# Performance work log

Measured on AMD Instinct MI355X. Metric: run time of the kernel, lower is better.

The kernel has to match this reference:

```python
import jax, jax.numpy as jnp
import numpy as np

G = 4          # num_groups == num_kv_groups


def _proj(W, b, xf):
    # 1x1 Conv3d == per-voxel linear: xf is [b, c, N]
    return jnp.einsum('oc,bcn->bon', W, xf) + b[None, :, None]


def setup_inputs() -> dict:
    key = jax.random.key(0)
    ks = jax.random.split(key, 5)
    c = 512
    x = jax.random.normal(ks[0], (2, c, 16, 16, 16), dtype=jnp.float32)
    s = 1.0 / np.sqrt(c)
    Wq = jax.random.normal(ks[1], (c, c), dtype=jnp.float32) * s
    Wk = jax.random.normal(ks[2], (c, c), dtype=jnp.float32) * s
    Wv = jax.random.normal(ks[3], (c, c), dtype=jnp.float32) * s
    Wo = jax.random.normal(ks[4], (c, c), dtype=jnp.float32) * s
    z = jnp.zeros((c,), dtype=jnp.float32)
    return {"x": x, "Wq": Wq, "bq": z, "Wk": Wk, "bk": z, "Wv": Wv, "bv": z, "Wo": Wo, "bo": z}


def reference(x, Wq, bq, Wk, bk, Wv, bv, Wo, bo):
    b, c, d, h, w = x.shape
    N = d * h * w
    gs = c // G                       # head (group) dim
    scale = gs ** -0.5
    xf = x.reshape(b, c, N)           # [b, c, N]
    q = _proj(Wq, bq, xf).reshape(b, G, gs, N).transpose(0, 1, 3, 2)  # [b,G,N,gs]
    k = _proj(Wk, bk, xf).reshape(b, G, gs, N).transpose(0, 1, 3, 2)
    v = _proj(Wv, bv, xf).reshape(b, G, gs, N).transpose(0, 1, 3, 2)
    sim = jnp.einsum('bgqd,bgkd->bgqk', q, k) * scale  # [b,G,N,N]
    attn = jax.nn.softmax(sim, axis=-1)
    out = jnp.einsum('bgqk,bgkd->bgqd', attn, v)       # [b,G,N,gs]
    out = out.transpose(0, 1, 3, 2).reshape(b, c, N)   # [b,c,N]
    out = _proj(Wo, bo, out).reshape(b, c, d, h, w)
    return x + out
```

## Files before the change

kernel.cpp:

```cpp
#include <hip/hip_runtime.h>
#include <hip/hip_bf16.h>
#include <stdint.h>

#define B_ 2
#define C_ 512
#define G_ 4
#define D_ 128
#define N_ 4096

typedef __bf16 bf16;
typedef __bf16 bf16x8 __attribute__((ext_vector_type(8)));
typedef float  f32x4  __attribute__((ext_vector_type(4)));
typedef float  f32x16 __attribute__((ext_vector_type(16)));

#define MFMA   __builtin_amdgcn_mfma_f32_16x16x32_bf16
#define MFMA32 __builtin_amdgcn_mfma_f32_32x32x16_bf16

#define SWZ(row, c) ((((c) ^ (((row) >> 1) & 3)) << 4))

#define OFF_Q   (0u)
#define OFF_K   (8388608u)
#define OFF_VT  (16777216u)
#define OFF_XT  (25165824u)
#define OFF_WB  (33554432u)
#define OFF_OP  (35651584u)
#define OFF_ML  (52428800u)
#define WS_NEED_SPLIT (52953088u)

__device__ inline unsigned pk2(float a, float b) {
    union { bf16 h[2]; unsigned u; } t;
    t.h[0] = (bf16)a; t.h[1] = (bf16)b;
    return t.u;
}
__device__ inline void pl32(unsigned &a, unsigned &b) {
    asm volatile("v_permlane32_swap_b32 %0, %1" : "+v"(a), "+v"(b));
}
__device__ inline void gload16(const char* src, char* lds) {
    __builtin_amdgcn_global_load_lds(
        (const __attribute__((address_space(1))) unsigned*)src,
        (__attribute__((address_space(3))) unsigned*)lds, 16, 0, 0);
}

__global__ __launch_bounds__(256) void wcvt_kernel(const float* __restrict__ Wq,
                                                   const float* __restrict__ Wk,
                                                   const float* __restrict__ Wv,
                                                   const float* __restrict__ Wo,
                                                   bf16* __restrict__ out) {
    int m = blockIdx.y;
    const float* W = (m == 0) ? Wq : (m == 1) ? Wk : (m == 2) ? Wv : Wo;
    int i = (blockIdx.x * 256 + threadIdx.x) * 4;
    float4 v = *(const float4*)(W + i);
    union { bf16 h[4]; uint2 u; } pk;
    pk.h[0] = (bf16)v.x; pk.h[1] = (bf16)v.y; pk.h[2] = (bf16)v.z; pk.h[3] = (bf16)v.w;
    *(uint2*)(out + (size_t)m * (C_ * C_) + i) = pk.u;
}

__global__ __launch_bounds__(256) void xt_kernel(const float* __restrict__ x,
                                                 bf16* __restrict__ xT) {
    __shared__ bf16 t[64 * 80];
    int n0 = blockIdx.x * 64, c0 = blockIdx.y * 64, b = blockIdx.z;
    const float* xp = x + (size_t)b * C_ * N_;
#pragma unroll
    for (int i = 0; i < 16; ++i) {
        int idx = threadIdx.x + 256 * i;
        int cl = idx >> 6, nl = idx & 63;
        float v = xp[(size_t)(c0 + cl) * N_ + n0 + nl];
        t[nl * 80 + cl] = (bf16)v;
    }
    __syncthreads();
    bf16* xt = xT + ((size_t)b * N_ + n0) * C_ + c0;
#pragma unroll
    for (int i = 0; i < 2; ++i) {
        int id = threadIdx.x + 256 * i;
        int nl = id >> 3, c8 = (id & 7) * 8;
        *(uint4*)(xt + (size_t)nl * C_ + c8) = *(const uint4*)(t + nl * 80 + c8);
    }
}

__global__ __launch_bounds__(256) void qkv_kernel(const bf16* __restrict__ xT,
                                                  const bf16* __restrict__ WB,
                                                  const float* __restrict__ bq,
                                                  const float* __restrict__ bk,
                                                  const float* __restrict__ bv,
                                                  bf16* __restrict__ Q,
                                                  bf16* __restrict__ K,
                                                  bf16* __restrict__ Vt) {
    __shared__ char smem[32768];
    const int tid = threadIdx.x;
    const int w = tid >> 6, l = tid & 63;
    const int lr = l & 15, lg = l >> 4;
    const int wr = w >> 1, wc = w & 1;
    const int mat = blockIdx.z;
    const bf16* A = xT;
    const bf16* W = WB + (size_t)mat * (C_ * C_);
    const float* bias = (mat == 0) ? bq : (mat == 1) ? bk : bv;
    const int r0 = blockIdx.x * 128, o0 = blockIdx.y * 128;
    const float QSCALE = 0.08838834764831845f * 1.4426950408889634f;

    const char* srcA[2]; const char* srcB[2]; int dA[2], dB[2];
#pragma unroll
    for (int i = 0; i < 2; ++i) {
        int CL = tid + 256 * i, row = CL >> 2, c = CL & 3;
        srcA[i] = (const char*)(A + (size_t)(r0 + row) * C_) + SWZ(row, c);
        srcB[i] = (const char*)(W + (size_t)(o0 + row) * C_) + SWZ(row, c);
        dA[i] = CL << 4;
        dB[i] = 8192 + (CL << 4);
    }

    f32x4 z = {0.f, 0.f, 0.f, 0.f};
    f32x4 acc[4][4];
#pragma unroll
    for (int m = 0; m < 4; ++m)
#pragma unroll
        for (int n = 0; n < 4; ++n) acc[m][n] = z;

    auto STAGE = [&](int buf, int kt) {
        char* base = smem + buf * 16384;
        int kb = kt * 64;
#pragma unroll
        for (int i = 0; i < 2; ++i) {
            gload16(srcA[i] + kb, base + dA[i]);
            gload16(srcB[i] + kb, base + dB[i]);
        }
    };

    STAGE(0, 0);
    __syncthreads();
#pragma unroll 4
    for (int t = 0; t < 16; ++t) {
        int cur = t & 1;
        if (t < 15) STAGE(cur ^ 1, t + 1);
        char* Ab = smem + cur * 16384;
        char* Bb = Ab + 8192;
        bf16x8 af[4], bg_[4];
#pragma unroll
        for (int m = 0; m < 4; ++m) {
            int row = wr * 64 + m * 16 + lr;
            af[m] = *(const bf16x8*)(Ab + row * 64 + SWZ(row, lg));
        }
#pragma unroll
        for (int n = 0; n < 4; ++n) {
            int row = wc * 64 + n * 16 + lr;
            bg_[n] = *(const bf16x8*)(Bb + row * 64 + SWZ(row, lg));
        }
#pragma unroll
        for (int m = 0; m < 4; ++m)
#pragma unroll
            for (int n = 0; n < 4; ++n)
                acc[m][n] = MFMA(af[m], bg_[n], acc[m][n], 0, 0, 0);
        __syncthreads();
    }

#pragma unroll
    for (int n = 0; n < 4; ++n) {
        int o = o0 + wc * 64 + n * 16 + lr;
        float bs = bias[o];
        int g = o >> 7, d = o & 127;
#pragma unroll
        for (int m = 0; m < 4; ++m) {
            int row = r0 + wr * 64 + m * 16 + lg * 4;
            int b = row >> 12, nn = row & (N_ - 1);
            if (mat == 0) {
#pragma unroll
                for (int j = 0; j < 4; ++j)
                    Q[((size_t)(b * G_ + g) * N_ + nn + j) * D_ + d] =
                        (bf16)((acc[m][n][j] + bs) * QSCALE);
            } else if (mat == 1) {
#pragma unroll
                for (int j = 0; j < 4; ++j)
                    K[((size_t)(b * G_ + g) * N_ + nn + j) * D_ + d] =
                        (bf16)(acc[m][n][j] + bs);
            } else {
                union { bf16 h[4]; uint2 u; } pk;
#pragma unroll
                for (int j = 0; j < 4; ++j) pk.h[j] = (bf16)(acc[m][n][j] + bs);
                *(uint2*)(Vt + ((size_t)(b * G_ + g) * D_ + d) * N_ + nn) = pk.u;
            }
        }
    }
}

template<int SPLITS>
__global__ __launch_bounds__(256, 2) void attn_kernel(const bf16* __restrict__ Q,
                                                      const bf16* __restrict__ K,
                                                      const bf16* __restrict__ Vt,
                                                      bf16* __restrict__ XT,
                                                      bf16* __restrict__ Op,
                                                      float* __restrict__ ML) {
    __shared__ char smem[65536];
    const int tid = threadIdx.x;
    const int w = tid >> 6, l = tid & 63;
    const int l31 = l & 31, h = l >> 5;
    const int bg = blockIdx.y;
    const int sp = (SPLITS > 1) ? blockIdx.z : 0;
    const bf16* Qh = Q + (size_t)bg * N_ * D_;
    const char* Kh = (const char*)(K + (size_t)bg * N_ * D_);
    const char* Vh = (const char*)(Vt + (size_t)bg * D_ * N_);
    const int q0 = blockIdx.x * 128 + w * 32;
    const int kv0 = sp * (N_ / SPLITS);
    const int NT = N_ / SPLITS / 64;

    int offK[4], offV[4];
#pragma unroll
    for (int j = 0; j < 4; ++j) {
        int CL = (w * 4 + j) * 64 + l;
        int row = CL >> 4;
        int cp = (CL & 15) ^ (row & 15);
        offK[j] = row * 256 + cp * 16;
        int dv = 2 * row + (cp >> 3), k8 = cp & 7;
        offV[j] = dv * (N_ * 2) + k8 * 16;
    }

    bf16x8 aq[8];
#pragma unroll
    for (int kb = 0; kb < 8; ++kb)
        aq[kb] = *(const bf16x8*)(Qh + (size_t)(q0 + l31) * D_ + kb * 16 + h * 8);

    f32x16 oacc[4];
#pragma unroll
    for (int dt = 0; dt < 4; ++dt)
#pragma unroll
        for (int r = 0; r < 16; ++r) oacc[dt][r] = 0.f;
    float mrun = -1e30f, lrun = 0.f;
    const float THR = 5.0f;

    auto STAGE = [&](int buf, int kv) {
        const char* pk = Kh + (size_t)kv * 256;
        const char* pv = Vh + (size_t)kv * 2;
        char* kb = smem + buf * 32768 + w * 4096;
        char* vb = smem + buf * 32768 + 16384 + w * 4096;
#pragma unroll
        for (int j = 0; j < 4; ++j) gload16(pk + offK[j], kb + j * 1024);
#pragma unroll
        for (int j = 0; j < 4; ++j) gload16(pv + offV[j], vb + j * 1024);
    };

    STAGE(0, kv0);
    __syncthreads();

    for (int t = 0; t < NT; ++t) {
        int cur = t & 1;
        if (t + 1 < NT) STAGE(cur ^ 1, kv0 + (t + 1) * 64);
        char* Kb = smem + cur * 32768;
        char* Vb = smem + cur * 32768 + 16384;

        f32x16 s0, s1;
#pragma unroll
        for (int r = 0; r < 16; ++r) { s0[r] = 0.f; s1[r] = 0.f; }
        __builtin_amdgcn_s_setprio(1);
#pragma unroll
        for (int kb = 0; kb < 8; ++kb) {
            int ch = (((kb << 1) | h) ^ (l31 & 15)) << 4;
            bf16x8 kf0 = *(const bf16x8*)(Kb + (size_t)l31 * 256 + ch);
            s0 = MFMA32(kf0, aq[kb], s0, 0, 0, 0);
            bf16x8 kf1 = *(const bf16x8*)(Kb + (size_t)(32 + l31) * 256 + ch);
            s1 = MFMA32(kf1, aq[kb], s1, 0, 0, 0);
        }
        __builtin_amdgcn_s_setprio(0);

        float m0 = fmaxf(s0[0], s1[0]), m1 = fmaxf(s0[1], s1[1]);
        float m2 = fmaxf(s0[2], s1[2]), m3 = fmaxf(s0[3], s1[3]);
#pragma unroll
        for (int r = 4; r < 16; r += 4) {
            m0 = fmaxf(m0, fmaxf(s0[r], s1[r]));
            m1 = fmaxf(m1, fmaxf(s0[r + 1], s1[r + 1]));
            m2 = fmaxf(m2, fmaxf(s0[r + 2], s1[r + 2]));
            m3 = fmaxf(m3, fmaxf(s0[r + 3], s1[r + 3]));
        }
        float mt = fmaxf(fmaxf(m0, m1), fmaxf(m2, m3));
        mt = fmaxf(mt, __shfl_xor(mt, 32));

        if (__any(mt > mrun + THR)) {
            float mn = fmaxf(mrun, mt);
            float corr = __builtin_amdgcn_exp2f(mrun - mn);
            mrun = mn; lrun *= corr;
#pragma unroll
            for (int r = 0; r < 16; ++r) {
                int qr = (r & 3) + 8 * (r >> 2) + 4 * h;
                float cr = __shfl(corr, qr);
#pragma unroll
                for (int dt = 0; dt < 4; ++dt) oacc[dt][r] *= cr;
            }
        }

        float a0 = 0.f, a1 = 0.f, a2 = 0.f, a3 = 0.f;
#pragma unroll
        for (int r = 0; r < 16; r += 4) {
            s0[r]     = __builtin_amdgcn_exp2f(s0[r] - mrun);     a0 += s0[r];
            s0[r + 1] = __builtin_amdgcn_exp2f(s0[r + 1] - mrun); a1 += s0[r + 1];
            s0[r + 2] = __builtin_amdgcn_exp2f(s0[r + 2] - mrun); a2 += s0[r + 2];
            s0[r + 3] = __builtin_amdgcn_exp2f(s0[r + 3] - mrun); a3 += s0[r + 3];
            s1[r]     = __builtin_amdgcn_exp2f(s1[r] - mrun);     a0 += s1[r];
            s1[r + 1] = __builtin_amdgcn_exp2f(s1[r + 1] - mrun); a1 += s1[r + 1];
            s1[r + 2] = __builtin_amdgcn_exp2f(s1[r + 2] - mrun); a2 += s1[r + 2];
            s1[r + 3] = __builtin_amdgcn_exp2f(s1[r + 3] - mrun); a3 += s1[r + 3];
        }
        float rs = (a0 + a1) + (a2 + a3);
        rs += __shfl_xor(rs, 32);
        lrun += rs;

        bf16x8 pa0, pa1, pa2, pa3;
        {
            unsigned x0 = pk2(s0[0], s0[1]),  y0 = pk2(s0[4], s0[5]);  pl32(x0, y0);
            unsigned x1 = pk2(s0[2], s0[3]),  y1 = pk2(s0[6], s0[7]);  pl32(x1, y1);
            pa0 = __builtin_bit_cast(bf16x8, (uint4){x0, x1, y0, y1});
            unsigned x2 = pk2(s0[8], s0[9]),  y2 = pk2(s0[12], s0[13]); pl32(x2, y2);
            unsigned x3 = pk2(s0[10], s0[11]), y3 = pk2(s0[14], s0[15]); pl32(x3, y3);
            pa1 = __builtin_bit_cast(bf16x8, (uint4){x2, x3, y2, y3});
            unsigned x4 = pk2(s1[0], s1[1]),  y4 = pk2(s1[4], s1[5]);  pl32(x4, y4);
            unsigned x5 = pk2(s1[2], s1[3]),  y5 = pk2(s1[6], s1[7]);  pl32(x5, y5);
            pa2 = __builtin_bit_cast(bf16x8, (uint4){x4, x5, y4, y5});
            unsigned x6 = pk2(s1[8], s1[9]),  y6 = pk2(s1[12], s1[13]); pl32(x6, y6);
            unsigned x7 = pk2(s1[10], s1[11]), y7 = pk2(s1[14], s1[15]); pl32(x7, y7);
            pa3 = __builtin_bit_cast(bf16x8, (uint4){x6, x7, y6, y7});
        }

        __builtin_amdgcn_s_setprio(1);
#pragma unroll
        for (int sl = 0; sl < 4; ++sl) {
            bf16x8 pa = (sl == 0) ? pa0 : (sl == 1) ? pa1 : (sl == 2) ? pa2 : pa3;
#pragma unroll
            for (int dt = 0; dt < 4; ++dt) {
                int row = dt * 16 + (l31 >> 1);
                int ch = ((((l31 & 1) << 3) + (sl << 1) + h) ^ (l31 >> 1)) << 4;
                bf16x8 vf = *(const bf16x8*)(Vb + (size_t)row * 256 + ch);
                oacc[dt] = MFMA32(pa, vf, oacc[dt], 0, 0, 0);
            }
        }
        __builtin_amdgcn_s_setprio(0);
        __syncthreads();
    }

    if (SPLITS > 1) {
        if (l < 32) {
            float2* mlp = (float2*)ML;
            float2 v; v.x = mrun; v.y = lrun;
            mlp[((size_t)sp * 8 + bg) * N_ + q0 + l31] = v;
        }
        bf16* op = Op + (((size_t)sp * 8 + bg) * N_ + q0) * D_;
#pragma unroll
        for (int dt = 0; dt < 4; ++dt)
#pragma unroll
            for (int r = 0; r < 16; ++r) {
                int qr = (r & 3) + 8 * (r >> 2) + 4 * h;
                op[(size_t)qr * D_ + dt * 32 + l31] = (bf16)oacc[dt][r];
            }
    } else {
        float linv = 1.f / lrun;
        int b = bg >> 2, g = bg & 3;
#pragma unroll
        for (int dt = 0; dt < 4; ++dt)
#pragma unroll
            for (int r = 0; r < 16; ++r) {
                int qr = (r & 3) + 8 * (r >> 2) + 4 * h;
                float sc = __shfl(linv, qr);
                XT[((size_t)b * N_ + q0 + qr) * C_ + g * D_ + dt * 32 + l31] =
                    (bf16)(oacc[dt][r] * sc);
            }
    }
}

__global__ __launch_bounds__(256) void merge_kernel(const bf16* __restrict__ Op,
                                                    const float* __restrict__ ML,
                                                    bf16* __restrict__ XT) {
    int t = threadIdx.x & 15, rl = threadIdx.x >> 4;
    int r = blockIdx.x * 16 + rl;
    int bg = r >> 12, n = r & (N_ - 1);
    const float2* mlp = (const float2*)ML;
    float2 ml0 = mlp[r], ml1 = mlp[32768 + r];
    float mm = fmaxf(ml0.x, ml1.x);
    float w0 = __builtin_amdgcn_exp2f(ml0.x - mm);
    float w1 = __builtin_amdgcn_exp2f(ml1.x - mm);
    float inv = 1.f / (w0 * ml0.y + w1 * ml1.y);
    w0 *= inv; w1 *= inv;
    bf16x8 o0 = *(const bf16x8*)(Op + (size_t)r * D_ + t * 8);
    bf16x8 o1 = *(const bf16x8*)(Op + (size_t)(32768 + r) * D_ + t * 8);
    union { bf16 h[8]; uint4 u; } pk;
#pragma unroll
    for (int e = 0; e < 8; ++e)
        pk.h[e] = (bf16)(w0 * (float)o0[e] + w1 * (float)o1[e]);
    int b = bg >> 2, g = bg & 3;
    *(uint4*)(XT + ((size_t)b * N_ + n) * C_ + g * D_ + t * 8) = pk.u;
}

__global__ __launch_bounds__(256) void oproj_kernel(const bf16* __restrict__ Ob,
                                                    const bf16* __restrict__ WB,
                                                    const float* __restrict__ bo,
                                                    const float* __restrict__ x,
                                                    float* __restrict__ out) {
    __shared__ char smem[24576];
    const int tid = threadIdx.x;
    const int w = tid >> 6, l = tid & 63;
    const int lr = l & 15, lg = l >> 4;
    const int wr = w >> 1, wc = w & 1;
    const bf16* W = WB + (size_t)3 * (C_ * C_);
    const int r0 = blockIdx.x * 128, o0 = blockIdx.y * 64;

    const char* srcA[2]; int dA[2];
#pragma unroll
    for (int i = 0; i < 2; ++i) {
        int CL = tid + 256 * i, row = CL >> 2, c = CL & 3;
        srcA[i] = (const char*)(Ob + (size_t)(r0 + row) * C_) + SWZ(row, c);
        dA[i] = CL << 4;
    }
    const char* srcB; int dB;
    {
        int CL = tid, row = CL >> 2, c = CL & 3;
        srcB = (const char*)(W + (size_t)(o0 + row) * C_) + SWZ(row, c);
        dB = 8192 + (CL << 4);
    }

    f32x4 z = {0.f, 0.f, 0.f, 0.f};
    f32x4 acc[4][2];
#pragma unroll
    for (int m = 0; m < 4; ++m) { acc[m][0] = z; acc[m][1] = z; }

    auto STAGE = [&](int buf, int kt) {
        char* base = smem + buf * 12288;
        int kb = kt * 64;
#pragma unroll
        for (int i = 0; i < 2; ++i) gload16(srcA[i] + kb, base + dA[i]);
        gload16(srcB + kb, base + dB);
    };

    STAGE(0, 0);
    __syncthreads();
#pragma unroll 4
    for (int t = 0; t < 16; ++t) {
        int cur = t & 1;
        if (t < 15) STAGE(cur ^ 1, t + 1);
        char* Ab = smem + cur * 12288;
        char* Bb = Ab + 8192;
        bf16x8 af[4], bg_[2];
#pragma unroll
        for (int m = 0; m < 4; ++m) {
            int row = wr * 64 + m * 16 + lr;
            af[m] = *(const bf16x8*)(Ab + row * 64 + SWZ(row, lg));
        }
#pragma unroll
        for (int n = 0; n < 2; ++n) {
            int row = wc * 32 + n * 16 + lr;
            bg_[n] = *(const bf16x8*)(Bb + row * 64 + SWZ(row, lg));
        }
#pragma unroll
        for (int m = 0; m < 4; ++m)
#pragma unroll
            for (int n = 0; n < 2; ++n)
                acc[m][n] = MFMA(af[m], bg_[n], acc[m][n], 0, 0, 0);
        __syncthreads();
    }

#pragma unroll
    for (int n = 0; n < 2; ++n) {
        int o = o0 + wc * 32 + n * 16 + lr;
        float bs = bo[o];
#pragma unroll
        for (int m = 0; m < 4; ++m) {
            int row = r0 + wr * 64 + m * 16 + lg * 4;
            int b = row >> 12, nn = row & (N_ - 1);
            size_t base = ((size_t)b * C_ + o) * N_ + nn;
            float4 xv = *(const float4*)(x + base);
            float4 ov;
            ov.x = acc[m][n][0] + bs + xv.x;
            ov.y = acc[m][n][1] + bs + xv.y;
            ov.z = acc[m][n][2] + bs + xv.z;
            ov.w = acc[m][n][3] + bs + xv.w;
            *(float4*)(out + base) = ov;
        }
    }
}

extern "C" void kernel_launch(void* const* d_in, const int* in_sizes, int n_in,
                              void* d_out, int out_size, void* d_ws, size_t ws_size,
                              hipStream_t stream) {
    const float* x  = (const float*)d_in[0];
    const float* Wq = (const float*)d_in[1];
    const float* bq = (const float*)d_in[2];
    const float* Wk = (const float*)d_in[3];
    const float* bk = (const float*)d_in[4];
    const float* Wv = (const float*)d_in[5];
    const float* bv = (const float*)d_in[6];
    const float* Wo = (const float*)d_in[7];
    const float* bo = (const float*)d_in[8];

    char* ws = (char*)d_ws;
    bf16* Q   = (bf16*)(ws + OFF_Q);
    bf16* K   = (bf16*)(ws + OFF_K);
    bf16* Vt  = (bf16*)(ws + OFF_VT);
    bf16* XT  = (bf16*)(ws + OFF_XT);
    bf16* WB  = (bf16*)(ws + OFF_WB);
    bf16* Op  = (bf16*)(ws + OFF_OP);
    float* ML = (float*)(ws + OFF_ML);
    float* out = (float*)d_out;

    hipLaunchKernelGGL(wcvt_kernel, dim3(256, 4), dim3(256), 0, stream, Wq, Wk, Wv, Wo, WB);
    hipLaunchKernelGGL(xt_kernel, dim3(64, 8, 2), dim3(256), 0, stream, x, XT);
    hipLaunchKernelGGL(qkv_kernel, dim3(64, 4, 3), dim3(256), 0, stream,
                       XT, WB, bq, bk, bv, Q, K, Vt);
    if (ws_size >= (size_t)WS_NEED_SPLIT) {
        hipLaunchKernelGGL(attn_kernel<2>, dim3(32, 8, 2), dim3(256), 0, stream,
                           Q, K, Vt, XT, Op, ML);
        hipLaunchKernelGGL(merge_kernel, dim3(2048), dim3(256), 0, stream, Op, ML, XT);
    } else {
        hipLaunchKernelGGL(attn_kernel<1>, dim3(32, 8, 1), dim3(256), 0, stream,
                           Q, K, Vt, XT, Op, ML);
    }
    hipLaunchKernelGGL(oproj_kernel, dim3(64, 8), dim3(256), 0, stream, XT, WB, bo, x, out);
}
```

Before: 140.6 us.

## Halve attention KV tile, raise occupancy, and add 4-way KV split with generic merge

The attention kernel now processes 32 KV rows per step instead of 64. LDS drops to 32 KB and launch bounds rise to 4 blocks per CU, and the V staging layout and swizzle are reworked to match. A 4-way split-KV path with a templated merge kernel is added when the workspace is large enough, which doubles the grid. The aim is more occupancy and parallelism to hide latency. The cost is more loop iterations, fewer MFMAs per softmax step, and extra partial-output traffic plus a heavier merge.

```diff
diff --git a/kernel.cpp b/kernel.cpp
--- a/kernel.cpp
+++ b/kernel.cpp
@@ -24,8 +24,8 @@
 #define OFF_XT  (25165824u)
 #define OFF_WB  (33554432u)
 #define OFF_OP  (35651584u)
-#define OFF_ML  (52428800u)
-#define WS_NEED_SPLIT (52953088u)
+#define WS_NEED2 (52953088u)
+#define WS_NEED4 (70254592u)
 
 __device__ inline unsigned pk2(float a, float b) {
     union { bf16 h[2]; unsigned u; } t;
@@ -181,13 +181,13 @@
 }
 
 template<int SPLITS>
-__global__ __launch_bounds__(256, 2) void attn_kernel(const bf16* __restrict__ Q,
+__global__ __launch_bounds__(256, 4) void attn_kernel(const bf16* __restrict__ Q,
                                                       const bf16* __restrict__ K,
                                                       const bf16* __restrict__ Vt,
                                                       bf16* __restrict__ XT,
                                                       bf16* __restrict__ Op,
                                                       float* __restrict__ ML) {
-    __shared__ char smem[65536];
+    __shared__ char smem[32768];
     const int tid = threadIdx.x;
     const int w = tid >> 6, l = tid & 63;
     const int l31 = l & 31, h = l >> 5;
@@ -198,17 +198,17 @@
     const char* Vh = (const char*)(Vt + (size_t)bg * D_ * N_);
     const int q0 = blockIdx.x * 128 + w * 32;
     const int kv0 = sp * (N_ / SPLITS);
-    const int NT = N_ / SPLITS / 64;
-
-    int offK[4], offV[4];
-#pragma unroll
-    for (int j = 0; j < 4; ++j) {
-        int CL = (w * 4 + j) * 64 + l;
+    const int NT = N_ / SPLITS / 32;
+
+    int offK[2], offV[2];
+#pragma unroll
+    for (int j = 0; j < 2; ++j) {
+        int CL = (w * 2 + j) * 64 + l;
         int row = CL >> 4;
         int cp = (CL & 15) ^ (row & 15);
         offK[j] = row * 256 + cp * 16;
-        int dv = 2 * row + (cp >> 3), k8 = cp & 7;
-        offV[j] = dv * (N_ * 2) + k8 * 16;
+        int dv = 4 * row + (cp >> 2), kvc = cp & 3;
+        offV[j] = dv * (N_ * 2) + kvc * 16;
     }
 
     bf16x8 aq[8];
@@ -227,12 +227,12 @@
     auto STAGE = [&](int buf, int kv) {
         const char* pk = Kh + (size_t)kv * 256;
         const char* pv = Vh + (size_t)kv * 2;
-        char* kb = smem + buf * 32768 + w * 4096;
-        char* vb = smem + buf * 32768 + 16384 + w * 4096;
-#pragma unroll
-        for (int j = 0; j < 4; ++j) gload16(pk + offK[j], kb + j * 1024);
-#pragma unroll
-        for (int j = 0; j < 4; ++j) gload16(pv + offV[j], vb + j * 1024);
+        char* kb = smem + buf * 16384 + w * 2048;
+        char* vb = smem + buf * 16384 + 8192 + w * 2048;
+#pragma unroll
+        for (int j = 0; j < 2; ++j) gload16(pk + offK[j], kb + j * 1024);
+#pragma unroll
+        for (int j = 0; j < 2; ++j) gload16(pv + offV[j], vb + j * 1024);
     };
 
     STAGE(0, kv0);
@@ -240,33 +240,28 @@
 
     for (int t = 0; t < NT; ++t) {
         int cur = t & 1;
-        if (t + 1 < NT) STAGE(cur ^ 1, kv0 + (t + 1) * 64);
-        char* Kb = smem + cur * 32768;
-        char* Vb = smem + cur * 32768 + 16384;
-
-        f32x16 s0, s1;
-#pragma unroll
-        for (int r = 0; r < 16; ++r) { s0[r] = 0.f; s1[r] = 0.f; }
+        if (t + 1 < NT) STAGE(cur ^ 1, kv0 + (t + 1) * 32);
+        char* Kb = smem + cur * 16384;
+        char* Vb = smem + cur * 16384 + 8192;
+
+        f32x16 s0;
+#pragma unroll
+        for (int r = 0; r < 16; ++r) s0[r] = 0.f;
         __builtin_amdgcn_s_setprio(1);
 #pragma unroll
         for (int kb = 0; kb < 8; ++kb) {
             int ch = (((kb << 1) | h) ^ (l31 & 15)) << 4;
             bf16x8 kf0 = *(const bf16x8*)(Kb + (size_t)l31 * 256 + ch);
             s0 = MFMA32(kf0, aq[kb], s0, 0, 0, 0);
-            bf16x8 kf1 = *(const bf16x8*)(Kb + (size_t)(32 + l31) * 256 + ch);
-            s1 = MFMA32(kf1, aq[kb], s1, 0, 0, 0);
         }
         __builtin_amdgcn_s_setprio(0);
 
-        float m0 = fmaxf(s0[0], s1[0]), m1 = fmaxf(s0[1], s1[1]);
-        float m2 = fmaxf(s0[2], s1[2]), m3 = fmaxf(s0[3], s1[3]);
-#pragma unroll
-        for (int r = 4; r < 16; r += 4) {
-            m0 = fmaxf(m0, fmaxf(s0[r], s1[r]));
-            m1 = fmaxf(m1, fmaxf(s0[r + 1], s1[r + 1]));
-            m2 = fmaxf(m2, fmaxf(s0[r + 2], s1[r + 2]));
-            m3 = fmaxf(m3, fmaxf(s0[r + 3], s1[r + 3]));
-        }
+        float m0 = fmaxf(s0[0], s0[4]), m1 = fmaxf(s0[1], s0[5]);
+        float m2 = fmaxf(s0[2], s0[6]), m3 = fmaxf(s0[3], s0[7]);
+        m0 = fmaxf(m0, fmaxf(s0[8], s0[12]));
+        m1 = fmaxf(m1, fmaxf(s0[9], s0[13]));
+        m2 = fmaxf(m2, fmaxf(s0[10], s0[14]));
+        m3 = fmaxf(m3, fmaxf(s0[11], s0[15]));
         float mt = fmaxf(fmaxf(m0, m1), fmaxf(m2, m3));
         mt = fmaxf(mt, __shfl_xor(mt, 32));
 
@@ -290,16 +285,12 @@
             s0[r + 1] = __builtin_amdgcn_exp2f(s0[r + 1] - mrun); a1 += s0[r + 1];
             s0[r + 2] = __builtin_amdgcn_exp2f(s0[r + 2] - mrun); a2 += s0[r + 2];
             s0[r + 3] = __builtin_amdgcn_exp2f(s0[r + 3] - mrun); a3 += s0[r + 3];
-            s1[r]     = __builtin_amdgcn_exp2f(s1[r] - mrun);     a0 += s1[r];
-            s1[r + 1] = __builtin_amdgcn_exp2f(s1[r + 1] - mrun); a1 += s1[r + 1];
-            s1[r + 2] = __builtin_amdgcn_exp2f(s1[r + 2] - mrun); a2 += s1[r + 2];
-            s1[r + 3] = __builtin_amdgcn_exp2f(s1[r + 3] - mrun); a3 += s1[r + 3];
         }
         float rs = (a0 + a1) + (a2 + a3);
         rs += __shfl_xor(rs, 32);
         lrun += rs;
 
-        bf16x8 pa0, pa1, pa2, pa3;
+        bf16x8 pa0, pa1;
         {
             unsigned x0 = pk2(s0[0], s0[1]),  y0 = pk2(s0[4], s0[5]);  pl32(x0, y0);
             unsigned x1 = pk2(s0[2], s0[3]),  y1 = pk2(s0[6], s0[7]);  pl32(x1, y1);
@@ -307,23 +298,17 @@
             unsigned x2 = pk2(s0[8], s0[9]),  y2 = pk2(s0[12], s0[13]); pl32(x2, y2);
             unsigned x3 = pk2(s0[10], s0[11]), y3 = pk2(s0[14], s0[15]); pl32(x3, y3);
             pa1 = __builtin_bit_cast(bf16x8, (uint4){x2, x3, y2, y3});
-            unsigned x4 = pk2(s1[0], s1[1]),  y4 = pk2(s1[4], s1[5]);  pl32(x4, y4);
-            unsigned x5 = pk2(s1[2], s1[3]),  y5 = pk2(s1[6], s1[7]);  pl32(x5, y5);
-            pa2 = __builtin_bit_cast(bf16x8, (uint4){x4, x5, y4, y5});
-            unsigned x6 = pk2(s1[8], s1[9]),  y6 = pk2(s1[12], s1[13]); pl32(x6, y6);
-            unsigned x7 = pk2(s1[10], s1[11]), y7 = pk2(s1[14], s1[15]); pl32(x7, y7);
-            pa3 = __builtin_bit_cast(bf16x8, (uint4){x6, x7, y6, y7});
         }
 
         __builtin_amdgcn_s_setprio(1);
 #pragma unroll
-        for (int sl = 0; sl < 4; ++sl) {
-            bf16x8 pa = (sl == 0) ? pa0 : (sl == 1) ? pa1 : (sl == 2) ? pa2 : pa3;
+        for (int sl = 0; sl < 2; ++sl) {
+            bf16x8 pa = (sl == 0) ? pa0 : pa1;
 #pragma unroll
             for (int dt = 0; dt < 4; ++dt) {
-                int row = dt * 16 + (l31 >> 1);
-                int ch = ((((l31 & 1) << 3) + (sl << 1) + h) ^ (l31 >> 1)) << 4;
-                bf16x8 vf = *(const bf16x8*)(Vb + (size_t)row * 256 + ch);
+                int rr = dt * 8 + (l31 >> 2);
+                int ch = ((((l31 & 3) << 2) + (sl << 1) + h) ^ (rr & 15)) << 4;
+                bf16x8 vf = *(const bf16x8*)(Vb + (size_t)rr * 256 + ch);
                 oacc[dt] = MFMA32(pa, vf, oacc[dt], 0, 0, 0);
             }
         }
@@ -360,6 +345,7 @@
     }
 }
 
+template<int NS>
 __global__ __launch_bounds__(256) void merge_kernel(const bf16* __restrict__ Op,
                                                     const float* __restrict__ ML,
                                                     bf16* __restrict__ XT) {
@@ -367,18 +353,27 @@
     int r = blockIdx.x * 16 + rl;
     int bg = r >> 12, n = r & (N_ - 1);
     const float2* mlp = (const float2*)ML;
-    float2 ml0 = mlp[r], ml1 = mlp[32768 + r];
-    float mm = fmaxf(ml0.x, ml1.x);
-    float w0 = __builtin_amdgcn_exp2f(ml0.x - mm);
-    float w1 = __builtin_amdgcn_exp2f(ml1.x - mm);
-    float inv = 1.f / (w0 * ml0.y + w1 * ml1.y);
-    w0 *= inv; w1 *= inv;
-    bf16x8 o0 = *(const bf16x8*)(Op + (size_t)r * D_ + t * 8);
-    bf16x8 o1 = *(const bf16x8*)(Op + (size_t)(32768 + r) * D_ + t * 8);
+    float2 ml[NS];
+    float mm = -1e30f;
+#pragma unroll
+    for (int s = 0; s < NS; ++s) { ml[s] = mlp[(size_t)s * 32768 + r]; mm = fmaxf(mm, ml[s].x); }
+    float ws[NS], den = 0.f;
+#pragma unroll
+    for (int s = 0; s < NS; ++s) { ws[s] = __builtin_amdgcn_exp2f(ml[s].x - mm); den += ws[s] * ml[s].y; }
+    float inv = 1.f / den;
+    float acc[8];
+#pragma unroll
+    for (int e = 0; e < 8; ++e) acc[e] = 0.f;
+#pragma unroll
+    for (int s = 0; s < NS; ++s) {
+        bf16x8 o = *(const bf16x8*)(Op + ((size_t)s * 32768 + r) * D_ + t * 8);
+        float wgt = ws[s] * inv;
+#pragma unroll
+        for (int e = 0; e < 8; ++e) acc[e] += wgt * (float)o[e];
+    }
     union { bf16 h[8]; uint4 u; } pk;
 #pragma unroll
-    for (int e = 0; e < 8; ++e)
-        pk.h[e] = (bf16)(w0 * (float)o0[e] + w1 * (float)o1[e]);
+    for (int e = 0; e < 8; ++e) pk.h[e] = (bf16)acc[e];
     int b = bg >> 2, g = bg & 3;
     *(uint4*)(XT + ((size_t)b * N_ + n) * C_ + g * D_ + t * 8) = pk.u;
 }
@@ -490,20 +485,25 @@
     bf16* XT  = (bf16*)(ws + OFF_XT);
     bf16* WB  = (bf16*)(ws + OFF_WB);
     bf16* Op  = (bf16*)(ws + OFF_OP);
-    float* ML = (float*)(ws + OFF_ML);
     float* out = (float*)d_out;
 
     hipLaunchKernelGGL(wcvt_kernel, dim3(256, 4), dim3(256), 0, stream, Wq, Wk, Wv, Wo, WB);
     hipLaunchKernelGGL(xt_kernel, dim3(64, 8, 2), dim3(256), 0, stream, x, XT);
     hipLaunchKernelGGL(qkv_kernel, dim3(64, 4, 3), dim3(256), 0, stream,
                        XT, WB, bq, bk, bv, Q, K, Vt);
-    if (ws_size >= (size_t)WS_NEED_SPLIT) {
+    if (ws_size >= (size_t)WS_NEED4) {
+        float* ML = (float*)(ws + OFF_OP + 4u * 8388608u);
+        hipLaunchKernelGGL(attn_kernel<4>, dim3(32, 8, 4), dim3(256), 0, stream,
+                           Q, K, Vt, XT, Op, ML);
+        hipLaunchKernelGGL(merge_kernel<4>, dim3(2048), dim3(256), 0, stream, Op, ML, XT);
+    } else if (ws_size >= (size_t)WS_NEED2) {
+        float* ML = (float*)(ws + OFF_OP + 2u * 8388608u);
         hipLaunchKernelGGL(attn_kernel<2>, dim3(32, 8, 2), dim3(256), 0, stream,
                            Q, K, Vt, XT, Op, ML);
-        hipLaunchKernelGGL(merge_kernel, dim3(2048), dim3(256), 0, stream, Op, ML, XT);
+        hipLaunchKernelGGL(merge_kernel<2>, dim3(2048), dim3(256), 0, stream, Op, ML, XT);
     } else {
         hipLaunchKernelGGL(attn_kernel<1>, dim3(32, 8, 1), dim3(256), 0, stream,
-                           Q, K, Vt, XT, Op, ML);
+                           Q, K, Vt, XT, Op, (float*)(ws + OFF_OP));
     }
     hipLaunchKernelGGL(oproj_kernel, dim3(64, 8), dim3(256), 0, stream, XT, WB, bo, x, out);
 }
```

New measurement: 281.4 us. 2x slower.
